# Performance work log

Hardware: AMD Instinct MI355X
Metric: run time of the kernel (lower is better)

Reference implementation:

```python
import jax, jax.numpy as jnp
import numpy as np

E, N, HID, NH = 250000, 50000, 128, 4
HD = HID // NH  # head_dim = 32


def setup_inputs() -> dict:
    key = jax.random.key(0)
    ks = jax.random.split(key, 16)
    f = lambda k, s: jax.random.normal(k, s, dtype=jnp.float32)
    w = lambda k, s: jax.random.normal(k, s, dtype=jnp.float32) * 0.05
    return {
        "edge_attr": f(ks[0], (E, HID)),
        "node_features": f(ks[1], (N, HID)),
        "regime_probs": jax.random.uniform(ks[2], (3,), dtype=jnp.float32),
        # phase_query / phase_key: Linear(hidden+3 -> hidden)
        "Wq": w(ks[3], (HID, HID + 3)), "bq": jnp.zeros((HID,), jnp.float32),
        "Wk": w(ks[4], (HID, HID + 3)), "bk": jnp.zeros((HID,), jnp.float32),
        # phase_value: Linear(hidden -> hidden)
        "Wv": w(ks[5], (HID, HID)), "bv": jnp.zeros((HID,), jnp.float32),
        # nn.MultiheadAttention packed in-projection [3*hid, hid] and out_proj
        "W_in": w(ks[6], (3 * HID, HID)), "b_in": jnp.zeros((3 * HID,), jnp.float32),
        "W_mo": w(ks[7], (HID, HID)), "b_mo": jnp.zeros((HID,), jnp.float32),
        # output_proj
        "Wo": w(ks[8], (HID, HID)), "bo": jnp.zeros((HID,), jnp.float32),
        "edge_index": jax.random.randint(ks[9], (2, E), 0, N, dtype=jnp.int64),
    }


def reference(edge_attr, node_features, regime_probs,
              Wq, bq, Wk, bk, Wv, bv,
              W_in, b_in, W_mo, b_mo, Wo, bo,
              edge_index):
    e = edge_attr.shape[0]
    src = node_features[edge_index[0]]  # [E, HID] gather
    tgt = node_features[edge_index[1]]  # [E, HID] gather
    reg = jnp.broadcast_to(regime_probs, (e, regime_probs.shape[0]))  # [E, 3]

    q = jnp.concatenate([src, reg], axis=1) @ Wq.T + bq  # [E, HID]
    k = jnp.concatenate([tgt, reg], axis=1) @ Wk.T + bk  # [E, HID]
    v = edge_attr @ Wv.T + bv                             # [E, HID]

    # nn.MultiheadAttention with seq_len 1 (batch_first): in-proj, heads, softmax, out-proj
    Wiq, Wik, Wiv = jnp.split(W_in, 3, axis=0)
    biq, bik, biv = jnp.split(b_in, 3)
    q2 = (q @ Wiq.T + biq).reshape(e, NH, HD)
    k2 = (k @ Wik.T + bik).reshape(e, NH, HD)
    v2 = (v @ Wiv.T + biv).reshape(e, NH, HD)

    scale = 1.0 / jnp.sqrt(jnp.float32(HD))
    scores = jnp.sum(q2 * k2, axis=-1, keepdims=True) * scale  # [E, NH, 1]
    probs = jax.nn.softmax(scores, axis=-1)                    # seq-len-1 -> all ones
    att = (probs * v2).reshape(e, HID)                         # == v2 merged
    att = att @ W_mo.T + b_mo                                  # MHA out_proj

    out = att @ Wo.T + bo                                      # output_proj
    return edge_attr + 0.5 * out
```

## Files before the change

kernel.cpp:

```cpp
#include <hip/hip_runtime.h>
#include <hip/hip_bf16.h>

#define HID 128

typedef __attribute__((ext_vector_type(8))) short short8;
typedef __attribute__((ext_vector_type(4))) float f32x4;

static __device__ __forceinline__ short f2bf(float x) {
    __hip_bfloat16 h = __float2bfloat16(x);
    return *reinterpret_cast<short*>(&h);
}

__global__ void prep_products(const float* __restrict__ Wo,
                              const float* __restrict__ W_mo,
                              const float* __restrict__ Wiv,
                              const float* __restrict__ Wv,
                              const float* __restrict__ bv,
                              const float* __restrict__ biv,
                              const float* __restrict__ b_mo,
                              const float* __restrict__ bo,
                              float* __restrict__ Pl,
                              float* __restrict__ Pr,
                              float* __restrict__ cv)
{
    const int j = threadIdx.x;
    const int b = blockIdx.x;
    __shared__ float sh[HID];

    if (b < 256) {
        const float* A = (b < 128) ? Wo   : Wiv;
        const float* B = (b < 128) ? W_mo : Wv;
        float*       C = (b < 128) ? Pl   : Pr;
        const int i = b & 127;
        sh[j] = A[i * HID + j];
        __syncthreads();
        float s = 0.f;
        #pragma unroll 16
        for (int k = 0; k < HID; ++k) s += sh[k] * B[k * HID + j];
        C[i * HID + j] = s;
    } else {
        sh[j] = bv[j];
        __syncthreads();
        float t = biv[j];
        #pragma unroll 16
        for (int k = 0; k < HID; ++k) t += Wiv[j * HID + k] * sh[k];
        __syncthreads(); sh[j] = t; __syncthreads();
        t = b_mo[j];
        #pragma unroll 16
        for (int k = 0; k < HID; ++k) t += W_mo[j * HID + k] * sh[k];
        __syncthreads(); sh[j] = t; __syncthreads();
        t = bo[j];
        #pragma unroll 16
        for (int k = 0; k < HID; ++k) t += Wo[j * HID + k] * sh[k];
        cv[j] = 0.5f * t;
    }
}

__global__ void prep_final(const float* __restrict__ Pl,
                           const float* __restrict__ Pr,
                           __hip_bfloat16* __restrict__ Mb)
{
    const int i = blockIdx.x, j = threadIdx.x;
    __shared__ float sh[HID];
    sh[j] = Pl[i * HID + j];
    __syncthreads();
    float s = 0.f;
    #pragma unroll 16
    for (int k = 0; k < HID; ++k) s += sh[k] * Pr[k * HID + j];
    Mb[i * HID + j] = __float2bfloat16(((i == j) ? 1.0f : 0.0f) + 0.5f * s);
}

__global__ __launch_bounds__(256) void edge_gemm(
    const float* __restrict__ ea,
    const __hip_bfloat16* __restrict__ Mb,
    const float* __restrict__ cvec,
    float* __restrict__ out,
    int E, int numTiles)
{
    __shared__ __align__(16) float lds[3][2048];

    const int lane  = threadIdx.x & 63;
    const int wv    = threadIdx.x >> 6;
    const int q     = lane >> 4;
    const int c     = lane & 15;
    const int ncol0 = wv * 32;

    short8 Mfrag[2][4];
    #pragma unroll
    for (int nt = 0; nt < 2; ++nt) {
        const __hip_bfloat16* mp = Mb + (size_t)(ncol0 + nt * 16 + c) * HID + q * 8;
        #pragma unroll
        for (int kk = 0; kk < 4; ++kk)
            Mfrag[nt][kk] = *reinterpret_cast<const short8*>(mp + kk * 32);
    }
    f32x4 cvp[2];
    #pragma unroll
    for (int nt = 0; nt < 2; ++nt)
        cvp[nt] = *reinterpret_cast<const f32x4*>(cvec + ncol0 + nt * 16 + q * 4);

    int t = blockIdx.x;
    if (t >= numTiles) return;
    const int G = gridDim.x;

    const int swz   = (c & 7) << 4;
    const int rbase = c * 512 + ((q * 32) ^ (swz & 0x60));
    const int hx    = swz & 16;

    auto stage_tile = [&](float* ldsbuf, int edge0) {
        #pragma unroll
        for (int j = 0; j < 2; ++j) {
            const int i = wv * 2 + j;
            const int r = i * 2 + (lane >> 5);
            const int b = ((lane & 31) * 16) ^ ((r & 7) << 4);
            int grow = edge0 + r; if (grow > E - 1) grow = E - 1;
            const char* src = (const char*)ea + (size_t)grow * 512 + b;
            float* dst = ldsbuf + i * 256;
            __builtin_amdgcn_global_load_lds(
                (const __attribute__((address_space(1))) void*)src,
                (__attribute__((address_space(3))) void*)dst,
                16, 0, 0);
        }
    };

    stage_tile(&lds[0][0], t * 16);
    if (t + G < numTiles) stage_tile(&lds[1][0], (t + G) * 16);
    asm volatile("s_waitcnt vmcnt(0)" ::: "memory");
    __builtin_amdgcn_s_barrier();
    __builtin_amdgcn_sched_barrier(0);

    int cur = 0;
    while (true) {
        const int edge0 = t * 16;
        const bool has_next  = (t + G     < numTiles);
        const bool has_next2 = (t + 2 * G < numTiles);

        if (has_next2) {
            int nb = cur + 2; if (nb >= 3) nb -= 3;
            stage_tile(&lds[nb][0], (t + 2 * G) * 16);
        }

        const char* lb = (const char*)&lds[cur][0];
        short8 bfrag[4];
        #pragma unroll
        for (int kk = 0; kk < 4; ++kk) {
            const float4 f0 = *reinterpret_cast<const float4*>(lb + rbase + kk * 128 + hx);
            const float4 f1 = *reinterpret_cast<const float4*>(lb + rbase + kk * 128 + (16 ^ hx));
            short8 v;
            v[0] = f2bf(f0.x); v[1] = f2bf(f0.y); v[2] = f2bf(f0.z); v[3] = f2bf(f0.w);
            v[4] = f2bf(f1.x); v[5] = f2bf(f1.y); v[6] = f2bf(f1.z); v[7] = f2bf(f1.w);
            bfrag[kk] = v;
        }

        f32x4 acc[2] = { cvp[0], cvp[1] };
        #pragma unroll
        for (int kk = 0; kk < 4; ++kk) {
            acc[0] = __builtin_amdgcn_mfma_f32_16x16x32_bf16(Mfrag[0][kk], bfrag[kk], acc[0], 0, 0, 0);
            acc[1] = __builtin_amdgcn_mfma_f32_16x16x32_bf16(Mfrag[1][kk], bfrag[kk], acc[1], 0, 0, 0);
        }

        const int orow = edge0 + c;
        if (orow < E) {
            float* op = out + (size_t)orow * HID + ncol0 + q * 4;
            *reinterpret_cast<f32x4*>(op)      = acc[0];
            *reinterpret_cast<f32x4*>(op + 16) = acc[1];
        }

        if (!has_next) break;

        asm volatile("s_waitcnt vmcnt(4)" ::: "memory");
        __builtin_amdgcn_s_barrier();
        __builtin_amdgcn_sched_barrier(0);

        cur += 1; if (cur >= 3) cur -= 3;
        t += G;
    }
}

extern "C" void kernel_launch(void* const* d_in, const int* in_sizes, int n_in,
                              void* d_out, int out_size, void* d_ws, size_t ws_size,
                              hipStream_t stream) {
    const float* Wv   = (const float*)d_in[7];
    const float* bv   = (const float*)d_in[8];
    const float* W_in = (const float*)d_in[9];
    const float* b_in = (const float*)d_in[10];
    const float* W_mo = (const float*)d_in[11];
    const float* b_mo = (const float*)d_in[12];
    const float* Wo   = (const float*)d_in[13];
    const float* bo   = (const float*)d_in[14];
    const float* Wiv  = W_in + 2 * HID * HID;
    const float* biv  = b_in + 2 * HID;

    char* ws = (char*)d_ws;
    float*          Pl = (float*)(ws);
    float*          Pr = (float*)(ws + 65536);
    __hip_bfloat16* Mb = (__hip_bfloat16*)(ws + 131072);
    float*          cv = (float*)(ws + 163840);

    const int E = in_sizes[0] / HID;
    const int numTiles = (E + 15) / 16;
    const int grid = numTiles < 2048 ? numTiles : 2048;

    prep_products<<<dim3(257), dim3(HID), 0, stream>>>(
        Wo, W_mo, Wiv, Wv, bv, biv, b_mo, bo, Pl, Pr, cv);
    prep_final<<<dim3(HID), dim3(HID), 0, stream>>>(Pl, Pr, Mb);

    edge_gemm<<<dim3(grid), dim3(256), 0, stream>>>(
        (const float*)d_in[0], Mb, cv, (float*)d_out, E, numTiles);
}
```

Baseline: 281.1 us.

## Split edge tile staging between LDS DMA and register loads

Each 16-edge tile is now staged in two halves. Rows 0-7 still go through global_load_lds DMA, while rows 8-15 are loaded into registers and written to LDS one iteration later. Buffers rotate by pointer swap, and the loop is unrolled twice so the two register staging slots alternate. The aim is to spread global-load traffic over both load paths and reduce how long the DMA path stays in flight. In exchange it adds LDS writes from registers and relies on a hand-tuned vmcnt/lgkmcnt wait scheme, which is fragile for ordering.

```diff
diff --git a/kernel.cpp b/kernel.cpp
--- a/kernel.cpp
+++ b/kernel.cpp
@@ -102,45 +102,37 @@
     if (t >= numTiles) return;
     const int G = gridDim.x;
 
+    auto dma_half = [&](float* buf, int edge0) {
+        const int r = wv * 2 + (lane >> 5);
+        const int b = ((lane & 31) * 16) ^ ((r & 7) << 4);
+        int grow = edge0 + r; if (grow > E - 1) grow = E - 1;
+        const char* src = (const char*)ea + (size_t)grow * 512 + b;
+        float* dst = buf + wv * 256;
+        __builtin_amdgcn_global_load_lds(
+            (const __attribute__((address_space(1))) void*)src,
+            (__attribute__((address_space(3))) void*)dst,
+            16, 0, 0);
+    };
+
+    const int rrow = 8 + (threadIdx.x >> 5);
+    const int roff = (threadIdx.x & 31) * 16;
+    const int rwad = rrow * 512 + (roff ^ ((rrow & 7) << 4));
+
+    auto reg_load = [&](int edge0, float4& rr) {
+        int grow = edge0 + rrow; if (grow > E - 1) grow = E - 1;
+        rr = *reinterpret_cast<const float4*>((const char*)ea + (size_t)grow * 512 + roff);
+    };
+    auto reg_write = [&](float* buf, const float4& rr) {
+        *reinterpret_cast<float4*>((char*)buf + rwad) = rr;
+    };
+
     const int swz   = (c & 7) << 4;
     const int rbase = c * 512 + ((q * 32) ^ (swz & 0x60));
     const int hx    = swz & 16;
 
-    auto stage_tile = [&](float* ldsbuf, int edge0) {
-        #pragma unroll
-        for (int j = 0; j < 2; ++j) {
-            const int i = wv * 2 + j;
-            const int r = i * 2 + (lane >> 5);
-            const int b = ((lane & 31) * 16) ^ ((r & 7) << 4);
-            int grow = edge0 + r; if (grow > E - 1) grow = E - 1;
-            const char* src = (const char*)ea + (size_t)grow * 512 + b;
-            float* dst = ldsbuf + i * 256;
-            __builtin_amdgcn_global_load_lds(
-                (const __attribute__((address_space(1))) void*)src,
-                (__attribute__((address_space(3))) void*)dst,
-                16, 0, 0);
-        }
-    };
-
-    stage_tile(&lds[0][0], t * 16);
-    if (t + G < numTiles) stage_tile(&lds[1][0], (t + G) * 16);
-    asm volatile("s_waitcnt vmcnt(0)" ::: "memory");
-    __builtin_amdgcn_s_barrier();
-    __builtin_amdgcn_sched_barrier(0);
-
-    int cur = 0;
-    while (true) {
-        const int edge0 = t * 16;
-        const bool has_next  = (t + G     < numTiles);
-        const bool has_next2 = (t + 2 * G < numTiles);
-
-        if (has_next2) {
-            int nb = cur + 2; if (nb >= 3) nb -= 3;
-            stage_tile(&lds[nb][0], (t + 2 * G) * 16);
-        }
-
-        const char* lb = (const char*)&lds[cur][0];
-        short8 bfrag[4];
+    auto compute_store = [&](const float* buf, int tt) {
+        const char* lb = (const char*)buf;
+        f32x4 acc[2] = { cvp[0], cvp[1] };
         #pragma unroll
         for (int kk = 0; kk < 4; ++kk) {
             const float4 f0 = *reinterpret_cast<const float4*>(lb + rbase + kk * 128 + hx);
@@ -148,31 +140,56 @@
             short8 v;
             v[0] = f2bf(f0.x); v[1] = f2bf(f0.y); v[2] = f2bf(f0.z); v[3] = f2bf(f0.w);
             v[4] = f2bf(f1.x); v[5] = f2bf(f1.y); v[6] = f2bf(f1.z); v[7] = f2bf(f1.w);
-            bfrag[kk] = v;
+            acc[0] = __builtin_amdgcn_mfma_f32_16x16x32_bf16(Mfrag[0][kk], v, acc[0], 0, 0, 0);
+            acc[1] = __builtin_amdgcn_mfma_f32_16x16x32_bf16(Mfrag[1][kk], v, acc[1], 0, 0, 0);
         }
-
-        f32x4 acc[2] = { cvp[0], cvp[1] };
-        #pragma unroll
-        for (int kk = 0; kk < 4; ++kk) {
-            acc[0] = __builtin_amdgcn_mfma_f32_16x16x32_bf16(Mfrag[0][kk], bfrag[kk], acc[0], 0, 0, 0);
-            acc[1] = __builtin_amdgcn_mfma_f32_16x16x32_bf16(Mfrag[1][kk], bfrag[kk], acc[1], 0, 0, 0);
-        }
-
-        const int orow = edge0 + c;
+        const int orow = tt * 16 + c;
         if (orow < E) {
             float* op = out + (size_t)orow * HID + ncol0 + q * 4;
             *reinterpret_cast<f32x4*>(op)      = acc[0];
             *reinterpret_cast<f32x4*>(op + 16) = acc[1];
         }
-
-        if (!has_next) break;
-
-        asm volatile("s_waitcnt vmcnt(4)" ::: "memory");
+    };
+
+    float* br = &lds[0][0];
+    float* bm = &lds[1][0];
+    float* bf = &lds[2][0];
+    float4 sA, sB;
+
+    dma_half(br, t * 16);
+    reg_load(t * 16, sA);
+    const bool h1p = (t + G < numTiles);
+    if (h1p) { dma_half(bm, (t + G) * 16); reg_load((t + G) * 16, sB); }
+    asm volatile("s_waitcnt vmcnt(0)" ::: "memory");
+    reg_write(br, sA);
+    asm volatile("s_waitcnt lgkmcnt(0)" ::: "memory");
+    __builtin_amdgcn_s_barrier();
+    __builtin_amdgcn_sched_barrier(0);
+
+    auto body = [&](float4& S, float4& So) -> bool {
+        const int t2g = t + 2 * G;
+        const bool has1 = (t + G < numTiles);
+        const bool has2 = (t2g < numTiles);
+
+        if (has2) { dma_half(bf, t2g * 16); reg_load(t2g * 16, S); }
+        if (has1) reg_write(bm, So);
+
+        asm volatile("s_waitcnt vmcnt(7)" ::: "memory");
+        asm volatile("s_waitcnt lgkmcnt(0)" ::: "memory");
         __builtin_amdgcn_s_barrier();
         __builtin_amdgcn_sched_barrier(0);
 
-        cur += 1; if (cur >= 3) cur -= 3;
+        compute_store(br, t);
+
+        if (!has1) return false;
+        float* tmp = br; br = bm; bm = bf; bf = tmp;
         t += G;
+        return true;
+    };
+
+    while (true) {
+        if (!body(sA, sB)) break;
+        if (!body(sB, sA)) break;
     }
 }
 
```

After: 282.3 us. Within noise of the previous version (+0.4%).
